# Performance work log

Measured on AMD Instinct MI355X. Metric: run time of the kernel, lower is better.

The kernel has to match this reference:

```python
import jax, jax.numpy as jnp
import numpy as np

EMB_DIM = 1024
ATTN_DIM = 1024


def setup_inputs() -> dict:
    key = jax.random.key(0)
    k_x, k_wk, k_wq, k_wv = jax.random.split(key, 4)
    bound = 1.0 / np.sqrt(EMB_DIM)  # nn.Linear default init range
    return {
        "embedded": jax.random.normal(k_x, (4, 2048, EMB_DIM), dtype=jnp.float32),
        "W_k": jax.random.uniform(k_wk, (ATTN_DIM, EMB_DIM), jnp.float32, -bound, bound),
        "W_q": jax.random.uniform(k_wq, (ATTN_DIM, EMB_DIM), jnp.float32, -bound, bound),
        "W_v": jax.random.uniform(k_wv, (ATTN_DIM, EMB_DIM), jnp.float32, -bound, bound),
    }


def reference(embedded, W_k, W_q, W_v):
    # Linear (bias=False): y = x @ W.T
    K = jnp.einsum("bse,ae->bsa", embedded, W_k)
    Q = jnp.einsum("bse,ae->bsa", embedded, W_q)
    V = jnp.einsum("bse,ae->bsa", embedded, W_v)
    S = K.shape[1]
    scale = 1.0 / jnp.sqrt(jnp.float32(ATTN_DIM))
    scores = jnp.einsum("bqa,bka->bqk", Q, K) * scale  # [B, S, S]
    causal = jnp.tril(jnp.ones((S, S), dtype=bool))  # True = keep
    scores = jnp.where(causal[None, :, :], scores, -jnp.inf)
    attn = jax.nn.softmax(scores, axis=2)
    out = jnp.einsum("bqk,bka->bqa", attn, V)
    # torch.round(x, decimals=4)
    return jnp.round(out * 1e4) / 1e4
```

## Files before the change

kernel.cpp:

```cpp
#include <hip/hip_runtime.h>
#include <stdint.h>

#define B_ 4
#define S_ 2048
#define E_ 1024
#define D_ 1024

typedef short  bf16x8 __attribute__((ext_vector_type(8)));
typedef float  f32x4  __attribute__((ext_vector_type(4)));

static __device__ __forceinline__ unsigned short f2bf(float f) {
    unsigned int u = __float_as_uint(f);
    u += 0x7fffu + ((u >> 16) & 1u);
    return (unsigned short)(u >> 16);
}

static __device__ __forceinline__ void async16(const unsigned short* g, unsigned short* l) {
    auto gp = (const __attribute__((address_space(1))) void*)(uintptr_t)g;
    auto lp = (__attribute__((address_space(3))) void*)(uintptr_t)l;
    __builtin_amdgcn_global_load_lds(gp, lp, 16, 0, 0);
}


__global__ __launch_bounds__(256)
void convert_kernel(const float* __restrict__ x,  const float* __restrict__ Wk,
                    const float* __restrict__ Wq, const float* __restrict__ Wv,
                    unsigned short* __restrict__ xb, unsigned short* __restrict__ Wb)
{
    const long long total  = (long long)B_ * S_ * E_ + 3LL * D_ * E_;
    const long long stride = (long long)gridDim.x * 256 * 4;
    for (long long idx = ((long long)blockIdx.x * 256 + threadIdx.x) * 4;
         idx < total; idx += stride) {
        const float* src; unsigned short* dst; long long off;
        if (idx < (long long)B_ * S_ * E_) {
            src = x; dst = xb; off = idx;
        } else {
            long long w = idx - (long long)B_ * S_ * E_;
            const int sel = (int)(w >> 20);
            off = w & 1048575LL;
            src = (sel == 0) ? Wk : (sel == 1) ? Wq : Wv;
            dst = Wb + ((long long)sel << 20);
        }
        const float4 f = *(const float4*)(src + off);
        ushort4 u = { f2bf(f.x), f2bf(f.y), f2bf(f.z), f2bf(f.w) };
        *(ushort4*)(dst + off) = u;
    }
}

__global__ __launch_bounds__(256, 4)
void proj_kernel(const unsigned short* __restrict__ xb,
                 const unsigned short* __restrict__ Wb,
                 unsigned short* __restrict__ Qb,
                 unsigned short* __restrict__ Kb,
                 unsigned short* __restrict__ Vt)
{
    __shared__ __align__(16) unsigned short As[128 * 64];
    __shared__ __align__(16) unsigned short Bs[128 * 64];

    const int t    = threadIdx.x;
    const int m0   = blockIdx.x * 128;
    const int ny   = blockIdx.y;
    const int wsel = ny >> 3;
    const int nloc = (ny & 7) * 128;

    const int lane = t & 63, wave = t >> 6;
    const int l15 = lane & 15, quad = lane >> 4;
    const int wm = wave & 1, wn = wave >> 1;
    const int sr = lane >> 3;
    const int sq = ((lane & 7) ^ sr) * 8;
    const int l7 = l15 & 7;
    const int rcA0 = (wm * 64 + l15) * 64 + ((quad ^ l7) * 8);
    const int rcA1 = (wm * 64 + l15) * 64 + (((4 + quad) ^ l7) * 8);
    const int rcB0 = (wn * 64 + l15) * 64 + ((quad ^ l7) * 8);
    const int rcB1 = (wn * 64 + l15) * 64 + (((4 + quad) ^ l7) * 8);

    const unsigned short* gA = xb + (size_t)(m0 + wave * 32 + sr) * E_ + sq;
    const unsigned short* gB = Wb + (size_t)(ny * 128 + wave * 32 + sr) * E_ + sq;
    unsigned short* lA = &As[wave * 2048];
    unsigned short* lB = &Bs[wave * 2048];

    f32x4 acc[4][4];
    #pragma unroll
    for (int i = 0; i < 4; i++)
        #pragma unroll
        for (int j = 0; j < 4; j++) acc[i][j] = {0.f, 0.f, 0.f, 0.f};

    for (int k0 = 0; k0 < E_; k0 += 64) {
        __syncthreads();
        #pragma unroll
        for (int i = 0; i < 4; i++) {
            async16(gA + k0 + i * 8 * E_, lA + i * 512);
            async16(gB + k0 + i * 8 * E_, lB + i * 512);
        }
        __syncthreads();

        #pragma unroll
        for (int s = 0; s < 2; s++) {
            bf16x8 af[4], bfr[4];
            const int ra = s ? rcA1 : rcA0, rb = s ? rcB1 : rcB0;
            #pragma unroll
            for (int i = 0; i < 4; i++) af[i]  = *(const bf16x8*)&As[ra + i * 1024];
            #pragma unroll
            for (int j = 0; j < 4; j++) bfr[j] = *(const bf16x8*)&Bs[rb + j * 1024];
            #pragma unroll
            for (int i = 0; i < 4; i++)
                #pragma unroll
                for (int j = 0; j < 4; j++)
                    acc[i][j] = __builtin_amdgcn_mfma_f32_16x16x32_bf16(af[i], bfr[j], acc[i][j], 0, 0, 0);
        }
    }

    if (wsel == 0) {
        #pragma unroll
        for (int i = 0; i < 4; i++)
            #pragma unroll
            for (int j = 0; j < 4; j++) {
                const int gn = nloc + wn * 64 + j * 16 + l15;
                #pragma unroll
                for (int r = 0; r < 4; r++) {
                    const int gm = m0 + wm * 64 + i * 16 + quad * 4 + r;
                    Kb[(size_t)gm * D_ + gn] = f2bf(acc[i][j][r]);
                }
            }
    } else if (wsel == 1) {
        #pragma unroll
        for (int i = 0; i < 4; i++)
            #pragma unroll
            for (int j = 0; j < 4; j++) {
                const int gn = nloc + wn * 64 + j * 16 + l15;
                #pragma unroll
                for (int r = 0; r < 4; r++) {
                    const int gm = m0 + wm * 64 + i * 16 + quad * 4 + r;
                    Qb[(size_t)gm * D_ + gn] = f2bf(acc[i][j][r] * 0.03125f);
                }
            }
    } else {
        #pragma unroll
        for (int i = 0; i < 4; i++)
            #pragma unroll
            for (int j = 0; j < 4; j++) {
                const int s0 = m0 + wm * 64 + i * 16 + quad * 4;
                const int b  = s0 >> 11, sl = s0 & (S_ - 1);
                const int gn = nloc + wn * 64 + j * 16 + l15;
                ushort4 u = { f2bf(acc[i][j][0]), f2bf(acc[i][j][1]),
                              f2bf(acc[i][j][2]), f2bf(acc[i][j][3]) };
                *(ushort4*)&Vt[((size_t)(b << 10) + gn) * S_ + sl] = u;
            }
    }
}

__global__ __launch_bounds__(256, 4)
void expscores_kernel(const unsigned short* __restrict__ Qb,
                      const unsigned short* __restrict__ Kb,
                      unsigned short* __restrict__ P,
                      float* __restrict__ rowpart)
{
    int rem = blockIdx.x;
    int mt = 15, cnt = 16;
    while (rem >= cnt) { rem -= cnt; mt--; cnt--; }
    const int nt = rem;
    const int b  = blockIdx.y;

    __shared__ __align__(16) unsigned short As[128 * 64];
    __shared__ __align__(16) unsigned short Bs[128 * 64];

    const int t = threadIdx.x;
    const int m0 = mt * 128, n0 = nt * 128;

    const int lane = t & 63, wave = t >> 6;
    const int l15 = lane & 15, quad = lane >> 4;
    const int wm = wave & 1, wn = wave >> 1;
    const int sr = lane >> 3;
    const int sq = ((lane & 7) ^ sr) * 8;
    const int l7 = l15 & 7;

    const unsigned short* gA = Qb + (size_t)b * S_ * D_ + (size_t)(m0 + wave * 32 + sr) * D_ + sq;
    const unsigned short* gB = Kb + (size_t)b * S_ * D_ + (size_t)(n0 + wave * 32 + sr) * D_ + sq;
    unsigned short* lA = &As[wave * 2048];
    unsigned short* lB = &Bs[wave * 2048];

    f32x4 acc[4][4];
    #pragma unroll
    for (int i = 0; i < 4; i++)
        #pragma unroll
        for (int j = 0; j < 4; j++) acc[i][j] = {0.f, 0.f, 0.f, 0.f};

    for (int kt = 0; kt < 16; kt++) {
        const int k0 = kt * 64;
        __syncthreads();
        #pragma unroll
        for (int i = 0; i < 4; i++) {
            async16(gA + k0 + i * 8 * D_, lA + i * 512);
            async16(gB + k0 + i * 8 * D_, lB + i * 512);
        }
        __syncthreads();

        #pragma unroll
        for (int s = 0; s < 2; s++) {
            const int cs = ((s * 4 + quad) ^ l7) * 8;
            bf16x8 af[4], bfr[4];
            #pragma unroll
            for (int i = 0; i < 4; i++)
                af[i] = *(const bf16x8*)&As[(wm * 64 + i * 16 + l15) * 64 + cs];
            #pragma unroll
            for (int j = 0; j < 4; j++)
                bfr[j] = *(const bf16x8*)&Bs[(wn * 64 + j * 16 + l15) * 64 + cs];
            #pragma unroll
            for (int i = 0; i < 4; i++)
                #pragma unroll
                for (int j = 0; j < 4; j++)
                    acc[i][j] = __builtin_amdgcn_mfma_f32_16x16x32_bf16(af[i], bfr[j], acc[i][j], 0, 0, 0);
        }
    }

    unsigned short* Pb = P + (size_t)b * S_ * S_;
    #pragma unroll
    for (int i = 0; i < 4; i++)
        #pragma unroll
        for (int j = 0; j < 4; j++) {
            const int gn = n0 + wn * 64 + j * 16 + l15;
            #pragma unroll
            for (int r = 0; r < 4; r++) {
                const int gm = m0 + wm * 64 + i * 16 + quad * 4 + r;
                const float e = (gn <= gm) ? __expf(acc[i][j][r]) : 0.f;
                acc[i][j][r] = e;
                Pb[(size_t)gm * S_ + gn] = f2bf(e);
            }
        }

    float* rp = rowpart + ((size_t)b * 32 + nt * 2 + wn) * S_;
    #pragma unroll
    for (int i = 0; i < 4; i++) {
        float rsub[4];
        #pragma unroll
        for (int r = 0; r < 4; r++) {
            float s = acc[i][0][r] + acc[i][1][r] + acc[i][2][r] + acc[i][3][r];
            #pragma unroll
            for (int off = 8; off; off >>= 1) s += __shfl_xor(s, off);
            rsub[r] = s;
        }
        if (l15 == 0) {
            #pragma unroll
            for (int r = 0; r < 4; r++)
                rp[m0 + wm * 64 + i * 16 + quad * 4 + r] = rsub[r];
        }
    }
}

__global__ __launch_bounds__(256, 2)
void pv_kernel(const unsigned short* __restrict__ P,
               const unsigned short* __restrict__ Vt,
               const float* __restrict__ rowpart,
               float* __restrict__ out)
{
    const int nt = blockIdx.x;
    const int yy = blockIdx.y;
    const int b  = blockIdx.z;
    const int mt = (b & 2) ? yy : (15 - yy);

    __shared__ __align__(16) unsigned short As[2 * 128 * 64];
    __shared__ __align__(16) unsigned short Bs[2 * 128 * 64];

    const int t = threadIdx.x;
    const int m0 = mt * 128, n0 = nt * 128;
    const int niter = 2 * mt + 2;

    const int lane = t & 63, wave = t >> 6;
    const int l15 = lane & 15, quad = lane >> 4;
    const int wm = wave & 1, wn = wave >> 1;
    const int sr = lane >> 3;
    const int sq = ((lane & 7) ^ sr) * 8;
    const int l7 = l15 & 7;

    const unsigned short* gA = P  + (size_t)b * S_ * S_ + (size_t)(m0 + wave * 32 + sr) * S_ + sq;
    const unsigned short* gB = Vt + (size_t)b * D_ * S_ + (size_t)(n0 + wave * 32 + sr) * S_ + sq;
    unsigned short* lA = &As[wave * 2048];
    unsigned short* lB = &Bs[wave * 2048];

    const float* rp = rowpart + (size_t)b * 32 * S_ + (m0 + wm * 64 + lane);
    float rsum = 0.f;
    for (int k = 0; k < niter; k++) rsum += rp[(size_t)k * S_];
    const float invr = 1.0f / rsum;

    f32x4 acc[4][4];
    #pragma unroll
    for (int i = 0; i < 4; i++)
        #pragma unroll
        for (int j = 0; j < 4; j++) acc[i][j] = {0.f, 0.f, 0.f, 0.f};

    #pragma unroll
    for (int i = 0; i < 4; i++) {
        async16(gA + i * 8 * S_, lA + i * 512);
        async16(gB + i * 8 * S_, lB + i * 512);
    }

    int buf = 0;
    for (int kt = 0; kt < niter; kt++) {
        __syncthreads();
        if (kt + 1 < niter) {
            const int k0 = (kt + 1) * 64;
            const int nb = (buf ^ 1) * 8192;
            #pragma unroll
            for (int i = 0; i < 4; i++) {
                async16(gA + k0 + i * 8 * S_, lA + nb + i * 512);
                async16(gB + k0 + i * 8 * S_, lB + nb + i * 512);
            }
        }
        const unsigned short* Ac = As + buf * 8192;
        const unsigned short* Bc = Bs + buf * 8192;
        #pragma unroll
        for (int s = 0; s < 2; s++) {
            const int cs = ((s * 4 + quad) ^ l7) * 8;
            bf16x8 af[4], bfr[4];
            #pragma unroll
            for (int i = 0; i < 4; i++)
                af[i] = *(const bf16x8*)&Ac[(wm * 64 + i * 16 + l15) * 64 + cs];
            #pragma unroll
            for (int j = 0; j < 4; j++)
                bfr[j] = *(const bf16x8*)&Bc[(wn * 64 + j * 16 + l15) * 64 + cs];
            #pragma unroll
            for (int i = 0; i < 4; i++)
                #pragma unroll
                for (int j = 0; j < 4; j++)
                    acc[i][j] = __builtin_amdgcn_mfma_f32_16x16x32_bf16(af[i], bfr[j], acc[i][j], 0, 0, 0);
        }
        buf ^= 1;
    }

    #pragma unroll
    for (int i = 0; i < 4; i++) {
        #pragma unroll
        for (int r = 0; r < 4; r++) {
            const float vr = __shfl(invr, i * 16 + quad * 4 + r);
            const int gm = m0 + wm * 64 + i * 16 + quad * 4 + r;
            #pragma unroll
            for (int j = 0; j < 4; j++) {
                const int gn = n0 + wn * 64 + j * 16 + l15;
                out[((size_t)b * S_ + gm) * D_ + gn] = rintf(acc[i][j][r] * vr * 1e4f) * 1e-4f;
            }
        }
    }
}

extern "C" void kernel_launch(void* const* d_in, const int* in_sizes, int n_in,
                              void* d_out, int out_size, void* d_ws, size_t ws_size,
                              hipStream_t stream)
{
    (void)in_sizes; (void)n_in; (void)out_size; (void)ws_size;
    const float* x  = (const float*)d_in[0];
    const float* Wk = (const float*)d_in[1];
    const float* Wq = (const float*)d_in[2];
    const float* Wv = (const float*)d_in[3];
    float* out = (float*)d_out;

    char* ws = (char*)d_ws;
    unsigned short* Qb = (unsigned short*)ws;
    unsigned short* Kb = Qb + (size_t)B_ * S_ * D_;
    unsigned short* Vt = Kb + (size_t)B_ * S_ * D_;
    unsigned short* P  = Vt + (size_t)B_ * D_ * S_;
    unsigned short* xb = P;
    unsigned short* Wb = xb + (size_t)B_ * S_ * E_;
    float* rowpart = (float*)(P + (size_t)B_ * S_ * S_);

    convert_kernel  <<<2048, 256, 0, stream>>>(x, Wk, Wq, Wv, xb, Wb);
    proj_kernel     <<<dim3(64, 24, 1),  256, 0, stream>>>(xb, Wb, Qb, Kb, Vt);
    expscores_kernel<<<dim3(136, B_, 1), 256, 0, stream>>>(Qb, Kb, P, rowpart);
    pv_kernel       <<<dim3(8, 16, B_),  256, 0, stream>>>(P, Vt, rowpart, out);
}
```

Before: 219.0 us.

## Rework QKV projection GEMM into 256x256 tiles with double-buffered LDS pipeline

The projection GEMM moves from 128x128 tiles with 256 threads and single-buffered LDS to 256x256 tiles with 512 threads. K-slices are double-buffered in 128 KB of dynamic LDS, and the next slice's async global-to-LDS loads are interleaved with MFMA work, using s_setprio and sub-step barriers. A block-index swizzle improves L2 locality. The aim is higher arithmetic intensity per LDS load and hiding global-load latency. In exchange, occupancy drops to one block per CU and register pressure rises.

```diff
diff --git a/kernel.cpp b/kernel.cpp
--- a/kernel.cpp
+++ b/kernel.cpp
@@ -47,101 +47,130 @@
     }
 }
 
-__global__ __launch_bounds__(256, 4)
+__global__ __launch_bounds__(512, 2)
 void proj_kernel(const unsigned short* __restrict__ xb,
                  const unsigned short* __restrict__ Wb,
                  unsigned short* __restrict__ Qb,
                  unsigned short* __restrict__ Kb,
                  unsigned short* __restrict__ Vt)
 {
-    __shared__ __align__(16) unsigned short As[128 * 64];
-    __shared__ __align__(16) unsigned short Bs[128 * 64];
-
-    const int t    = threadIdx.x;
-    const int m0   = blockIdx.x * 128;
-    const int ny   = blockIdx.y;
-    const int wsel = ny >> 3;
-    const int nloc = (ny & 7) * 128;
-
+    extern __shared__ __align__(16) unsigned short lds[];
+
+    const int bid = blockIdx.x;
+    const int swz = (bid & 7) * 48 + (bid >> 3);
+    const int my  = swz / 12;
+    const int ny  = swz - my * 12;
+    const int m0  = my * 256;
+    const int wsel = ny >> 2;
+    const int nloc = (ny & 3) * 256;
+
+    const int t = threadIdx.x;
     const int lane = t & 63, wave = t >> 6;
     const int l15 = lane & 15, quad = lane >> 4;
-    const int wm = wave & 1, wn = wave >> 1;
-    const int sr = lane >> 3;
-    const int sq = ((lane & 7) ^ sr) * 8;
+    const int wm2 = wave & 1, wn4 = wave >> 1;
+    const int lr = lane >> 3;
+    const int lc = ((lane & 7) ^ lr) * 8;
     const int l7 = l15 & 7;
-    const int rcA0 = (wm * 64 + l15) * 64 + ((quad ^ l7) * 8);
-    const int rcA1 = (wm * 64 + l15) * 64 + (((4 + quad) ^ l7) * 8);
-    const int rcB0 = (wn * 64 + l15) * 64 + ((quad ^ l7) * 8);
-    const int rcB1 = (wn * 64 + l15) * 64 + (((4 + quad) ^ l7) * 8);
-
-    const unsigned short* gA = xb + (size_t)(m0 + wave * 32 + sr) * E_ + sq;
-    const unsigned short* gB = Wb + (size_t)(ny * 128 + wave * 32 + sr) * E_ + sq;
-    unsigned short* lA = &As[wave * 2048];
-    unsigned short* lB = &Bs[wave * 2048];
-
-    f32x4 acc[4][4];
-    #pragma unroll
-    for (int i = 0; i < 4; i++)
+
+    const unsigned short* gAb = xb + (size_t)(m0 + lr) * E_ + lc;
+    const unsigned short* gBb = Wb + (size_t)(ny * 256 + lr) * E_ + lc;
+
+    f32x4 acc[8][4];
+    #pragma unroll
+    for (int i = 0; i < 8; i++)
         #pragma unroll
         for (int j = 0; j < 4; j++) acc[i][j] = {0.f, 0.f, 0.f, 0.f};
 
-    for (int k0 = 0; k0 < E_; k0 += 64) {
+    #pragma unroll
+    for (int i = 0; i < 8; i++) {
+        const int u = wave * 8 + i;
+        if (u < 32) async16(gAb + (size_t)(u * 8) * E_,        lds +         u * 512);
+        else        async16(gBb + (size_t)((u - 32) * 8) * E_, lds + 32768 + (u - 32) * 512);
+    }
+    __syncthreads();
+
+    for (int kt = 0; kt < 16; kt++) {
+        const int c = kt & 1;
+        const unsigned short* Ac = lds + c * 16384;
+        const unsigned short* Bc = lds + 32768 + c * 16384;
+        unsigned short* An = lds + (c ^ 1) * 16384;
+        unsigned short* Bn = lds + 32768 + (c ^ 1) * 16384;
+
+        #pragma unroll
+        for (int p = 0; p < 4; p++) {
+            if (kt < 15) {
+                const int k0 = (kt + 1) * 64;
+                #pragma unroll
+                for (int i = 0; i < 2; i++) {
+                    const int u = wave * 8 + p * 2 + i;
+                    if (u < 32) async16(gAb + (size_t)(u * 8) * E_ + k0,        An +        u * 512);
+                    else        async16(gBb + (size_t)((u - 32) * 8) * E_ + k0, Bn + (u - 32) * 512);
+                }
+            }
+            const int mh = p >> 1, nh = p & 1;
+            bf16x8 af[2][4], bfr[2][2];
+            #pragma unroll
+            for (int s = 0; s < 2; s++) {
+                const int cs = ((s * 4 + quad) ^ l7) * 8;
+                #pragma unroll
+                for (int ii = 0; ii < 4; ii++) {
+                    const int r = wm2 * 128 + (mh * 4 + ii) * 16 + l15;
+                    af[s][ii] = *(const bf16x8*)&Ac[r * 64 + cs];
+                }
+                #pragma unroll
+                for (int jj = 0; jj < 2; jj++) {
+                    const int r = wn4 * 64 + (nh * 2 + jj) * 16 + l15;
+                    bfr[s][jj] = *(const bf16x8*)&Bc[r * 64 + cs];
+                }
+            }
+            __builtin_amdgcn_s_setprio(1);
+            #pragma unroll
+            for (int s = 0; s < 2; s++)
+                #pragma unroll
+                for (int ii = 0; ii < 4; ii++)
+                    #pragma unroll
+                    for (int jj = 0; jj < 2; jj++)
+                        acc[mh * 4 + ii][nh * 2 + jj] =
+                            __builtin_amdgcn_mfma_f32_16x16x32_bf16(
+                                af[s][ii], bfr[s][jj], acc[mh * 4 + ii][nh * 2 + jj], 0, 0, 0);
+            __builtin_amdgcn_s_setprio(0);
+            if (p < 3) __builtin_amdgcn_s_barrier();
+        }
         __syncthreads();
-        #pragma unroll
-        for (int i = 0; i < 4; i++) {
-            async16(gA + k0 + i * 8 * E_, lA + i * 512);
-            async16(gB + k0 + i * 8 * E_, lB + i * 512);
-        }
-        __syncthreads();
-
-        #pragma unroll
-        for (int s = 0; s < 2; s++) {
-            bf16x8 af[4], bfr[4];
-            const int ra = s ? rcA1 : rcA0, rb = s ? rcB1 : rcB0;
-            #pragma unroll
-            for (int i = 0; i < 4; i++) af[i]  = *(const bf16x8*)&As[ra + i * 1024];
-            #pragma unroll
-            for (int j = 0; j < 4; j++) bfr[j] = *(const bf16x8*)&Bs[rb + j * 1024];
-            #pragma unroll
-            for (int i = 0; i < 4; i++)
-                #pragma unroll
-                for (int j = 0; j < 4; j++)
-                    acc[i][j] = __builtin_amdgcn_mfma_f32_16x16x32_bf16(af[i], bfr[j], acc[i][j], 0, 0, 0);
-        }
     }
 
     if (wsel == 0) {
         #pragma unroll
-        for (int i = 0; i < 4; i++)
+        for (int i = 0; i < 8; i++)
             #pragma unroll
             for (int j = 0; j < 4; j++) {
-                const int gn = nloc + wn * 64 + j * 16 + l15;
+                const int gn = nloc + wn4 * 64 + j * 16 + l15;
                 #pragma unroll
                 for (int r = 0; r < 4; r++) {
-                    const int gm = m0 + wm * 64 + i * 16 + quad * 4 + r;
+                    const int gm = m0 + wm2 * 128 + i * 16 + quad * 4 + r;
                     Kb[(size_t)gm * D_ + gn] = f2bf(acc[i][j][r]);
                 }
             }
     } else if (wsel == 1) {
         #pragma unroll
-        for (int i = 0; i < 4; i++)
+        for (int i = 0; i < 8; i++)
             #pragma unroll
             for (int j = 0; j < 4; j++) {
-                const int gn = nloc + wn * 64 + j * 16 + l15;
+                const int gn = nloc + wn4 * 64 + j * 16 + l15;
                 #pragma unroll
                 for (int r = 0; r < 4; r++) {
-                    const int gm = m0 + wm * 64 + i * 16 + quad * 4 + r;
+                    const int gm = m0 + wm2 * 128 + i * 16 + quad * 4 + r;
                     Qb[(size_t)gm * D_ + gn] = f2bf(acc[i][j][r] * 0.03125f);
                 }
             }
     } else {
         #pragma unroll
-        for (int i = 0; i < 4; i++)
+        for (int i = 0; i < 8; i++)
             #pragma unroll
             for (int j = 0; j < 4; j++) {
-                const int s0 = m0 + wm * 64 + i * 16 + quad * 4;
+                const int s0 = m0 + wm2 * 128 + i * 16 + quad * 4;
                 const int b  = s0 >> 11, sl = s0 & (S_ - 1);
-                const int gn = nloc + wn * 64 + j * 16 + l15;
+                const int gn = nloc + wn4 * 64 + j * 16 + l15;
                 ushort4 u = { f2bf(acc[i][j][0]), f2bf(acc[i][j][1]),
                               f2bf(acc[i][j][2]), f2bf(acc[i][j][3]) };
                 *(ushort4*)&Vt[((size_t)(b << 10) + gn) * S_ + sl] = u;
@@ -363,7 +392,7 @@
     float* rowpart = (float*)(P + (size_t)B_ * S_ * S_);
 
     convert_kernel  <<<2048, 256, 0, stream>>>(x, Wk, Wq, Wv, xb, Wb);
-    proj_kernel     <<<dim3(64, 24, 1),  256, 0, stream>>>(xb, Wb, Qb, Kb, Vt);
+    proj_kernel     <<<dim3(384, 1, 1), 512, 131072, stream>>>(xb, Wb, Qb, Kb, Vt);
     expscores_kernel<<<dim3(136, B_, 1), 256, 0, stream>>>(Qb, Kb, P, rowpart);
     pv_kernel       <<<dim3(8, 16, B_),  256, 0, stream>>>(P, Vt, rowpart, out);
 }
```

Measured after the change: 238.1 us. 8.7% more time.

## Double-buffer score GEMM and use partial vmcnt waits in both attention GEMMs

Applied to the files above, without the earlier changes.

The exp-scores kernel now double-buffers its Q/K tiles in LDS and prefetches the next k-tile before computing the current one, where before it loaded and then synchronized each step. Both it and the PV kernel replace __syncthreads with explicit s_waitcnt vmcnt(8) plus raw barriers and sched_barriers, so only the older group of async loads has to finish before compute starts. This aims to overlap global-to-LDS transfers with MFMA work. In exchange the score kernel uses twice the LDS and its occupancy hint drops from 4 to 2 blocks. The hand-written vmcnt counts also depend on the exact number of outstanding loads.

```diff
diff --git a/kernel.cpp b/kernel.cpp
--- a/kernel.cpp
+++ b/kernel.cpp
@@ -149,7 +149,7 @@
     }
 }
 
-__global__ __launch_bounds__(256, 4)
+__global__ __launch_bounds__(256, 2)
 void expscores_kernel(const unsigned short* __restrict__ Qb,
                       const unsigned short* __restrict__ Kb,
                       unsigned short* __restrict__ P,
@@ -161,8 +161,8 @@
     const int nt = rem;
     const int b  = blockIdx.y;
 
-    __shared__ __align__(16) unsigned short As[128 * 64];
-    __shared__ __align__(16) unsigned short Bs[128 * 64];
+    __shared__ __align__(16) unsigned short As[2 * 128 * 64];
+    __shared__ __align__(16) unsigned short Bs[2 * 128 * 64];
 
     const int t = threadIdx.x;
     const int m0 = mt * 128, n0 = nt * 128;
@@ -185,15 +185,28 @@
         #pragma unroll
         for (int j = 0; j < 4; j++) acc[i][j] = {0.f, 0.f, 0.f, 0.f};
 
+    #pragma unroll
+    for (int i = 0; i < 4; i++) {
+        async16(gA + i * 8 * D_, lA + i * 512);
+        async16(gB + i * 8 * D_, lB + i * 512);
+    }
+
     for (int kt = 0; kt < 16; kt++) {
-        const int k0 = kt * 64;
-        __syncthreads();
-        #pragma unroll
-        for (int i = 0; i < 4; i++) {
-            async16(gA + k0 + i * 8 * D_, lA + i * 512);
-            async16(gB + k0 + i * 8 * D_, lB + i * 512);
-        }
-        __syncthreads();
+        const int cb = (kt & 1) * 8192;
+        const int nb = ((kt & 1) ^ 1) * 8192;
+        if (kt < 15) {
+            const int k0 = (kt + 1) * 64;
+            #pragma unroll
+            for (int i = 0; i < 4; i++) {
+                async16(gA + k0 + i * 8 * D_, lA + nb + i * 512);
+                async16(gB + k0 + i * 8 * D_, lB + nb + i * 512);
+            }
+            asm volatile("s_waitcnt vmcnt(8)" ::: "memory");
+        } else {
+            asm volatile("s_waitcnt vmcnt(0)" ::: "memory");
+        }
+        __builtin_amdgcn_s_barrier();
+        __builtin_amdgcn_sched_barrier(0);
 
         #pragma unroll
         for (int s = 0; s < 2; s++) {
@@ -201,16 +214,19 @@
             bf16x8 af[4], bfr[4];
             #pragma unroll
             for (int i = 0; i < 4; i++)
-                af[i] = *(const bf16x8*)&As[(wm * 64 + i * 16 + l15) * 64 + cs];
+                af[i] = *(const bf16x8*)&As[cb + (wm * 64 + i * 16 + l15) * 64 + cs];
             #pragma unroll
             for (int j = 0; j < 4; j++)
-                bfr[j] = *(const bf16x8*)&Bs[(wn * 64 + j * 16 + l15) * 64 + cs];
+                bfr[j] = *(const bf16x8*)&Bs[cb + (wn * 64 + j * 16 + l15) * 64 + cs];
             #pragma unroll
             for (int i = 0; i < 4; i++)
                 #pragma unroll
                 for (int j = 0; j < 4; j++)
                     acc[i][j] = __builtin_amdgcn_mfma_f32_16x16x32_bf16(af[i], bfr[j], acc[i][j], 0, 0, 0);
         }
+
+        __builtin_amdgcn_sched_barrier(0);
+        __builtin_amdgcn_s_barrier();
     }
 
     unsigned short* Pb = P + (size_t)b * S_ * S_;
@@ -281,6 +297,7 @@
     float rsum = 0.f;
     for (int k = 0; k < niter; k++) rsum += rp[(size_t)k * S_];
     const float invr = 1.0f / rsum;
+    asm volatile("s_waitcnt vmcnt(0)" ::: "memory");
 
     f32x4 acc[4][4];
     #pragma unroll
@@ -294,37 +311,42 @@
         async16(gB + i * 8 * S_, lB + i * 512);
     }
 
-    int buf = 0;
     for (int kt = 0; kt < niter; kt++) {
-        __syncthreads();
+        const int cb = (kt & 1) * 8192;
+        const int nb = ((kt & 1) ^ 1) * 8192;
         if (kt + 1 < niter) {
             const int k0 = (kt + 1) * 64;
-            const int nb = (buf ^ 1) * 8192;
             #pragma unroll
             for (int i = 0; i < 4; i++) {
                 async16(gA + k0 + i * 8 * S_, lA + nb + i * 512);
                 async16(gB + k0 + i * 8 * S_, lB + nb + i * 512);
             }
-        }
-        const unsigned short* Ac = As + buf * 8192;
-        const unsigned short* Bc = Bs + buf * 8192;
+            asm volatile("s_waitcnt vmcnt(8)" ::: "memory");
+        } else {
+            asm volatile("s_waitcnt vmcnt(0)" ::: "memory");
+        }
+        __builtin_amdgcn_s_barrier();
+        __builtin_amdgcn_sched_barrier(0);
+
         #pragma unroll
         for (int s = 0; s < 2; s++) {
             const int cs = ((s * 4 + quad) ^ l7) * 8;
             bf16x8 af[4], bfr[4];
             #pragma unroll
             for (int i = 0; i < 4; i++)
-                af[i] = *(const bf16x8*)&Ac[(wm * 64 + i * 16 + l15) * 64 + cs];
+                af[i] = *(const bf16x8*)&As[cb + (wm * 64 + i * 16 + l15) * 64 + cs];
             #pragma unroll
             for (int j = 0; j < 4; j++)
-                bfr[j] = *(const bf16x8*)&Bc[(wn * 64 + j * 16 + l15) * 64 + cs];
+                bfr[j] = *(const bf16x8*)&Bs[cb + (wn * 64 + j * 16 + l15) * 64 + cs];
             #pragma unroll
             for (int i = 0; i < 4; i++)
                 #pragma unroll
                 for (int j = 0; j < 4; j++)
                     acc[i][j] = __builtin_amdgcn_mfma_f32_16x16x32_bf16(af[i], bfr[j], acc[i][j], 0, 0, 0);
         }
-        buf ^= 1;
+
+        __builtin_amdgcn_sched_barrier(0);
+        __builtin_amdgcn_s_barrier();
     }
 
     #pragma unroll
```

Measured after the change: 219.8 us. About the same (+0.3%).

## Fuse score and PV kernels into persistent grid with per-row-tile completion counters

Applied to the files above, without the earlier changes.

Merges the exp-scores and PV kernels into a single launch. PV blocks spin on atomic per-(batch,row-tile) counters, set by the score blocks, before consuming P, so PV work can overlap the tail of score computation and one launch boundary is removed. Because the merged kernel runs at 4 blocks per CU, PV loses its LDS double buffering and now uses a single buffer with two barriers per k-step. The spin-wait relies on producer blocks being scheduled ahead of dependent consumers, which the block ordering is meant to guarantee.

```diff
diff --git a/kernel.cpp b/kernel.cpp
--- a/kernel.cpp
+++ b/kernel.cpp
@@ -25,8 +25,11 @@
 __global__ __launch_bounds__(256)
 void convert_kernel(const float* __restrict__ x,  const float* __restrict__ Wk,
                     const float* __restrict__ Wq, const float* __restrict__ Wv,
-                    unsigned short* __restrict__ xb, unsigned short* __restrict__ Wb)
-{
+                    unsigned short* __restrict__ xb, unsigned short* __restrict__ Wb,
+                    int* __restrict__ done)
+{
+    if (blockIdx.x == 0 && threadIdx.x < 64) done[threadIdx.x] = 0;
+
     const long long total  = (long long)B_ * S_ * E_ + 3LL * D_ * E_;
     const long long stride = (long long)gridDim.x * 256 * 4;
     for (long long idx = ((long long)blockIdx.x * 256 + threadIdx.x) * 4;
@@ -149,20 +152,16 @@
     }
 }
 
-__global__ __launch_bounds__(256, 4)
-void expscores_kernel(const unsigned short* __restrict__ Qb,
-                      const unsigned short* __restrict__ Kb,
-                      unsigned short* __restrict__ P,
-                      float* __restrict__ rowpart)
-{
-    int rem = blockIdx.x;
+static __device__ __forceinline__
+void do_exp(int g, const unsigned short* Qb, const unsigned short* Kb,
+            unsigned short* P, float* rowpart, int* done,
+            unsigned short* As, unsigned short* Bs)
+{
+    const int b = g & 3;
+    int rem = g >> 2;
     int mt = 15, cnt = 16;
     while (rem >= cnt) { rem -= cnt; mt--; cnt--; }
     const int nt = rem;
-    const int b  = blockIdx.y;
-
-    __shared__ __align__(16) unsigned short As[128 * 64];
-    __shared__ __align__(16) unsigned short Bs[128 * 64];
 
     const int t = threadIdx.x;
     const int m0 = mt * 128, n0 = nt * 128;
@@ -245,25 +244,35 @@
                 rp[m0 + wm * 64 + i * 16 + quad * 4 + r] = rsub[r];
         }
     }
-}
-
-__global__ __launch_bounds__(256, 2)
-void pv_kernel(const unsigned short* __restrict__ P,
-               const unsigned short* __restrict__ Vt,
-               const float* __restrict__ rowpart,
-               float* __restrict__ out)
-{
-    const int nt = blockIdx.x;
-    const int yy = blockIdx.y;
-    const int b  = blockIdx.z;
-    const int mt = (b & 2) ? yy : (15 - yy);
-
-    __shared__ __align__(16) unsigned short As[2 * 128 * 64];
-    __shared__ __align__(16) unsigned short Bs[2 * 128 * 64];
-
-    const int t = threadIdx.x;
+
+    __syncthreads();
+    if (t == 0) {
+        __threadfence();
+        __hip_atomic_fetch_add(&done[b * 16 + mt], 1,
+                               __ATOMIC_RELEASE, __HIP_MEMORY_SCOPE_AGENT);
+    }
+}
+
+static __device__ __forceinline__
+void do_pv(int pid, const unsigned short* P, const unsigned short* Vt,
+           const float* rowpart, float* out, int* done,
+           unsigned short* As, unsigned short* Bs)
+{
+    const int mt  = 15 - (pid >> 5);
+    const int rem = pid & 31;
+    const int b   = rem >> 3;
+    const int nt  = rem & 7;
     const int m0 = mt * 128, n0 = nt * 128;
     const int niter = 2 * mt + 2;
+
+    const int t = threadIdx.x;
+    if (t == 0) {
+        while (__hip_atomic_load(&done[b * 16 + mt],
+                                 __ATOMIC_ACQUIRE, __HIP_MEMORY_SCOPE_AGENT) < mt + 1)
+            __builtin_amdgcn_s_sleep(8);
+        __threadfence();
+    }
+    __syncthreads();
 
     const int lane = t & 63, wave = t >> 6;
     const int l15 = lane & 15, quad = lane >> 4;
@@ -288,43 +297,32 @@
         #pragma unroll
         for (int j = 0; j < 4; j++) acc[i][j] = {0.f, 0.f, 0.f, 0.f};
 
-    #pragma unroll
-    for (int i = 0; i < 4; i++) {
-        async16(gA + i * 8 * S_, lA + i * 512);
-        async16(gB + i * 8 * S_, lB + i * 512);
-    }
-
-    int buf = 0;
     for (int kt = 0; kt < niter; kt++) {
-        __syncthreads();
-        if (kt + 1 < niter) {
-            const int k0 = (kt + 1) * 64;
-            const int nb = (buf ^ 1) * 8192;
-            #pragma unroll
-            for (int i = 0; i < 4; i++) {
-                async16(gA + k0 + i * 8 * S_, lA + nb + i * 512);
-                async16(gB + k0 + i * 8 * S_, lB + nb + i * 512);
-            }
-        }
-        const unsigned short* Ac = As + buf * 8192;
-        const unsigned short* Bc = Bs + buf * 8192;
+        const int k0 = kt * 64;
+        __syncthreads();
+        #pragma unroll
+        for (int i = 0; i < 4; i++) {
+            async16(gA + k0 + i * 8 * S_, lA + i * 512);
+            async16(gB + k0 + i * 8 * S_, lB + i * 512);
+        }
+        __syncthreads();
+
         #pragma unroll
         for (int s = 0; s < 2; s++) {
             const int cs = ((s * 4 + quad) ^ l7) * 8;
             bf16x8 af[4], bfr[4];
             #pragma unroll
             for (int i = 0; i < 4; i++)
-                af[i] = *(const bf16x8*)&Ac[(wm * 64 + i * 16 + l15) * 64 + cs];
+                af[i] = *(const bf16x8*)&As[(wm * 64 + i * 16 + l15) * 64 + cs];
             #pragma unroll
             for (int j = 0; j < 4; j++)
-                bfr[j] = *(const bf16x8*)&Bc[(wn * 64 + j * 16 + l15) * 64 + cs];
+                bfr[j] = *(const bf16x8*)&Bs[(wn * 64 + j * 16 + l15) * 64 + cs];
             #pragma unroll
             for (int i = 0; i < 4; i++)
                 #pragma unroll
                 for (int j = 0; j < 4; j++)
                     acc[i][j] = __builtin_amdgcn_mfma_f32_16x16x32_bf16(af[i], bfr[j], acc[i][j], 0, 0, 0);
         }
-        buf ^= 1;
     }
 
     #pragma unroll
@@ -339,6 +337,27 @@
                 out[((size_t)b * S_ + gm) * D_ + gn] = rintf(acc[i][j][r] * vr * 1e4f) * 1e-4f;
             }
         }
+    }
+}
+
+__global__ __launch_bounds__(256, 4)
+void attn_kernel(const unsigned short* __restrict__ Qb,
+                 const unsigned short* __restrict__ Kb,
+                 const unsigned short* __restrict__ Vt,
+                 unsigned short* __restrict__ P,
+                 float* __restrict__ rowpart,
+                 float* __restrict__ out,
+                 int* __restrict__ done)
+{
+    __shared__ __align__(16) unsigned short As[128 * 64];
+    __shared__ __align__(16) unsigned short Bs[128 * 64];
+
+    const int bid = blockIdx.x;
+    if (bid < 544) {
+        do_exp(bid, Qb, Kb, P, rowpart, done, As, Bs);
+        if (bid < 32) do_pv(480 + bid, P, Vt, rowpart, out, done, As, Bs);
+    } else {
+        do_pv(bid - 544, P, Vt, rowpart, out, done, As, Bs);
     }
 }
 
@@ -361,9 +380,9 @@
     unsigned short* xb = P;
     unsigned short* Wb = xb + (size_t)B_ * S_ * E_;
     float* rowpart = (float*)(P + (size_t)B_ * S_ * S_);
-
-    convert_kernel  <<<2048, 256, 0, stream>>>(x, Wk, Wq, Wv, xb, Wb);
-    proj_kernel     <<<dim3(64, 24, 1),  256, 0, stream>>>(xb, Wb, Qb, Kb, Vt);
-    expscores_kernel<<<dim3(136, B_, 1), 256, 0, stream>>>(Qb, Kb, P, rowpart);
-    pv_kernel       <<<dim3(8, 16, B_),  256, 0, stream>>>(P, Vt, rowpart, out);
-}
+    int* done = (int*)(rowpart + (size_t)B_ * 32 * S_);
+
+    convert_kernel<<<2048, 256, 0, stream>>>(x, Wk, Wq, Wv, xb, Wb, done);
+    proj_kernel   <<<dim3(64, 24, 1), 256, 0, stream>>>(xb, Wb, Qb, Kb, Vt);
+    attn_kernel   <<<dim3(1024, 1, 1), 256, 0, stream>>>(Qb, Kb, Vt, P, rowpart, out, done);
+}
```

Measured after the change: 348.5 us. 59.1% more time.
